# Kernel tuning notes

Hardware: AMD Instinct MI355X
Metric: run time of the kernel (lower is better)

Reference implementation:

```python
import jax, jax.numpy as jnp
import numpy as np

# ---- config (matches init_kwargs) ----
B, N, D = 16, 300, 256
HEADS, HD = 8, D // 8
FF = 1024
HID = FF // 2                      # SwiGLU hidden
SPATIAL = [(80, 80), (40, 40), (20, 20), (10, 10)]
LVL = len(SPATIAL)
NP = 4                              # points per level
TP = LVL * NP                       # total sampling points = 16
L = sum(h * w for h, w in SPATIAL)  # 8400
EPS = 1e-6


def setup_inputs() -> dict:
    key = jax.random.key(0)
    ks = jax.random.split(key, 24)
    s = 0.02
    return {
        "target": jax.random.normal(ks[0], (B, N, D), jnp.float32),
        "reference_points": jax.random.uniform(ks[1], (B, N, 1, 4), jnp.float32, 0.05, 0.95),
        "memory": jax.random.normal(ks[2], (B, L, D), jnp.float32),
        # self-attention
        "qkv_w": jax.random.normal(ks[3], (3 * D, D), jnp.float32) * s,
        "qkv_b": jnp.zeros((3 * D,), jnp.float32),
        "out_w": jax.random.normal(ks[4], (D, D), jnp.float32) * s,
        "out_b": jnp.zeros((D,), jnp.float32),
        "norm1_w": jnp.ones((D,), jnp.float32),
        # deformable cross-attention
        "off_w": jax.random.normal(ks[5], (HEADS * TP * 2, D), jnp.float32) * s,
        "off_b": jax.random.normal(ks[6], (HEADS * TP * 2,), jnp.float32) * 0.1,
        "aw_w": jax.random.normal(ks[7], (HEADS * TP, D), jnp.float32) * s,
        "aw_b": jnp.zeros((HEADS * TP,), jnp.float32),
        "cout_w": jax.random.normal(ks[8], (D, D), jnp.float32) * s,
        "cout_b": jnp.zeros((D,), jnp.float32),
        "norm2_w": jnp.ones((D,), jnp.float32),
        # SwiGLU FFN
        "w13": jax.random.normal(ks[9], (2 * HID, D), jnp.float32) * s,
        "w13_b": jnp.zeros((2 * HID,), jnp.float32),
        "w2": jax.random.normal(ks[10], (D, HID), jnp.float32) * s,
        "w2_b": jnp.zeros((D,), jnp.float32),
        "norm3_w": jnp.ones((D,), jnp.float32),
    }


def rmsnorm(x, w):
    return x * jax.lax.rsqrt(jnp.mean(x * x, axis=-1, keepdims=True) + EPS) * w


def bilinear_sample(vflat, loc, H, W):
    """vflat: (BH, hd, H*W); loc: (BH, Q, 2) in [0,1]. grid_sample align_corners=False, zero pad."""
    x = loc[..., 0] * W - 0.5
    y = loc[..., 1] * H - 0.5
    x0 = jnp.floor(x); y0 = jnp.floor(y)
    dx = x - x0; dy = y - y0
    x0i = x0.astype(jnp.int32); y0i = y0.astype(jnp.int32)

    def gather(xi, yi, w):
        valid = (xi >= 0) & (xi < W) & (yi >= 0) & (yi < H)
        idx = jnp.clip(yi, 0, H - 1) * W + jnp.clip(xi, 0, W - 1)
        g = jnp.take_along_axis(vflat, idx[:, None, :], axis=2)  # (BH, hd, Q)
        return g * (w * valid)[:, None, :]

    return (gather(x0i, y0i, (1 - dx) * (1 - dy))
            + gather(x0i + 1, y0i, dx * (1 - dy))
            + gather(x0i, y0i + 1, (1 - dx) * dy)
            + gather(x0i + 1, y0i + 1, dx * dy))


def reference(target, reference_points, memory, qkv_w, qkv_b, out_w, out_b, norm1_w,
              off_w, off_b, aw_w, aw_b, cout_w, cout_b, norm2_w,
              w13, w13_b, w2, w2_b, norm3_w):
    # ---------- self-attention (query_pos_embed=None, attn_mask=None) ----------
    qkv = target @ qkv_w.T + qkv_b                    # (B,N,3D)
    qkv = qkv.reshape(B, N, 3, HEADS, HD).transpose(2, 0, 3, 1, 4)
    q, k, v = qkv[0], qkv[1], qkv[2]                  # (B,H,N,hd)
    attn = jax.nn.softmax(jnp.einsum("bhqd,bhkd->bhqk", q, k) / np.sqrt(HD), axis=-1)
    sa = jnp.einsum("bhqk,bhkd->bhqd", attn, v).transpose(0, 2, 1, 3).reshape(B, N, D)
    x = rmsnorm(target + (sa @ out_w.T + out_b), norm1_w)

    # ---------- deformable cross-attention ----------
    # value_op: memory -> per-head value (B,H,hd,L)
    val = memory.reshape(B, L, HEADS, HD).transpose(0, 2, 3, 1).reshape(B * HEADS, HD, L)

    offsets = (x @ off_w.T + off_b).reshape(B, N, HEADS, TP, 2)
    aw = jax.nn.softmax((x @ aw_w.T + aw_b).reshape(B, N, HEADS, TP), axis=-1)

    ref_xy = reference_points[:, :, :, None, :2]      # (B,N,1,1,2)
    ref_wh = reference_points[:, :, :, None, 2:]
    pts_scale = 1.0 / NP
    loc = ref_xy + offsets * pts_scale * ref_wh * 0.5  # (B,N,H,TP,2)
    loc = loc.transpose(0, 2, 1, 3, 4).reshape(B * HEADS, N, TP, 2)

    sampled = []
    start = 0
    for li, (H, W) in enumerate(SPATIAL):
        v_l = jax.lax.dynamic_slice_in_dim(val, start, H * W, axis=2)
        loc_l = loc[:, :, li * NP:(li + 1) * NP, :].reshape(B * HEADS, N * NP, 2)
        s = bilinear_sample(v_l, loc_l, H, W).reshape(B * HEADS, HD, N, NP)
        sampled.append(s)
        start += H * W
    sampled = jnp.concatenate(sampled, axis=-1)        # (BH, hd, N, TP)

    w = aw.transpose(0, 2, 1, 3).reshape(B * HEADS, 1, N, TP)
    ca = (sampled * w).sum(-1)                         # (BH, hd, N)
    ca = ca.reshape(B, HEADS, HD, N).transpose(0, 3, 1, 2).reshape(B, N, D)
    ca = ca @ cout_w.T + cout_b

    x = rmsnorm(x + ca, norm2_w)

    # ---------- SwiGLU FFN ----------
    h = x @ w13.T + w13_b
    h1, h2 = h[..., :HID], h[..., HID:]
    ffn = (jax.nn.silu(h1) * h2) @ w2.T + w2_b
    x = jnp.clip(x + ffn, -65504.0, 65504.0)
    return rmsnorm(x, norm3_w)
```

## Files before the change

kernel.cpp:

```cpp
#include <hip/hip_runtime.h>
#include <cstdint>
#include <cstddef>


typedef __attribute__((ext_vector_type(8))) short bf16x8;
typedef __attribute__((ext_vector_type(4))) float f32x4;

__device__ __forceinline__ unsigned short f2bf(float f) {
  unsigned int u = __float_as_uint(f);
  u = (u + 0x7fffu + ((u >> 16) & 1u)) >> 16;
  return (unsigned short)u;
}
__device__ __forceinline__ unsigned int pack2bf(float lo, float hi) {
  return ((unsigned int)f2bf(hi) << 16) | (unsigned int)f2bf(lo);
}

__device__ __forceinline__ void gemm_dev(
    const float* __restrict__ A, const float* __restrict__ W,
    const float* __restrict__ bias, float* __restrict__ C,
    int N, int K, int row0, int col0,
    unsigned short* As, unsigned short* Ws)
{
  const int t = threadIdx.x, wave = t >> 6, lane = t & 63;
  const int lr = lane & 15, g = lane >> 4;
  const int sr = t >> 4, sc = (t & 15) * 4;

  float4 ra[4], rw[8];
  const float* Ab = A + (size_t)(row0 + sr) * K + sc;
  const float* Wb = W + (size_t)(col0 + sr) * K + sc;

#pragma unroll
  for (int i = 0; i < 4; ++i) ra[i] = *(const float4*)(Ab + (size_t)16 * i * K);
#pragma unroll
  for (int j = 0; j < 8; ++j) rw[j] = *(const float4*)(Wb + (size_t)16 * j * K);

  f32x4 acc[4][2] = {};

  for (int k0 = 0; k0 < K; k0 += 64) {
    __syncthreads();
#pragma unroll
    for (int i = 0; i < 4; ++i) {
      uint2 p;
      p.x = pack2bf(ra[i].x, ra[i].y);
      p.y = pack2bf(ra[i].z, ra[i].w);
      *(uint2*)&As[(sr + 16 * i) * 72 + sc] = p;
    }
#pragma unroll
    for (int j = 0; j < 8; ++j) {
      uint2 p;
      p.x = pack2bf(rw[j].x, rw[j].y);
      p.y = pack2bf(rw[j].z, rw[j].w);
      *(uint2*)&Ws[(sr + 16 * j) * 72 + sc] = p;
    }
    __syncthreads();

    if (k0 + 64 < K) {
#pragma unroll
      for (int i = 0; i < 4; ++i)
        ra[i] = *(const float4*)(Ab + (size_t)16 * i * K + k0 + 64);
#pragma unroll
      for (int j = 0; j < 8; ++j)
        rw[j] = *(const float4*)(Wb + (size_t)16 * j * K + k0 + 64);
    }

#pragma unroll
    for (int ks = 0; ks < 2; ++ks) {
      bf16x8 aA[4], bB[2];
#pragma unroll
      for (int i = 0; i < 4; ++i)
        aA[i] = *(const bf16x8*)&As[(i * 16 + lr) * 72 + ks * 32 + g * 8];
#pragma unroll
      for (int j = 0; j < 2; ++j)
        bB[j] = *(const bf16x8*)&Ws[(wave * 32 + j * 16 + lr) * 72 + ks * 32 + g * 8];
#pragma unroll
      for (int i = 0; i < 4; ++i)
#pragma unroll
        for (int j = 0; j < 2; ++j)
          acc[i][j] = __builtin_amdgcn_mfma_f32_16x16x32_bf16(aA[i], bB[j], acc[i][j], 0, 0, 0);
    }
  }

  const float b0 = bias[col0 + wave * 32 + lr];
  const float b1 = bias[col0 + wave * 32 + 16 + lr];
#pragma unroll
  for (int i = 0; i < 4; ++i) {
#pragma unroll
    for (int r = 0; r < 4; ++r) {
      const int row = row0 + i * 16 + g * 4 + r;
      float* dst = &C[(size_t)row * N + col0 + wave * 32 + lr];
      dst[0]  = acc[i][0][r] + b0;
      dst[16] = acc[i][1][r] + b1;
    }
  }
}

__global__ __launch_bounds__(256) void gemm_mfma(
    const float* __restrict__ A, const float* __restrict__ W,
    const float* __restrict__ bias, float* __restrict__ C, int N, int K)
{
  __shared__ __align__(16) unsigned short As[64 * 72];
  __shared__ __align__(16) unsigned short Ws[128 * 72];
  gemm_dev(A, W, bias, C, N, K, blockIdx.y * 64, blockIdx.x * 128, As, Ws);
}

__global__ __launch_bounds__(256) void gemm_offaw(
    const float* __restrict__ X,
    const float* __restrict__ off_w, const float* __restrict__ off_b, float* __restrict__ OF,
    const float* __restrict__ aw_w, const float* __restrict__ aw_b, float* __restrict__ AW,
    int K)
{
  __shared__ __align__(16) unsigned short As[64 * 72];
  __shared__ __align__(16) unsigned short Ws[128 * 72];
  if (blockIdx.x < 2)
    gemm_dev(X, off_w, off_b, OF, 256, K, blockIdx.y * 64, blockIdx.x * 128, As, Ws);
  else
    gemm_dev(X, aw_w, aw_b, AW, 128, K, blockIdx.y * 64, 0, As, Ws);
}

__global__ __launch_bounds__(256) void gemm_qkv(
    const float* __restrict__ A, const float* __restrict__ W,
    const float* __restrict__ bias,
    unsigned short* __restrict__ Qb, unsigned short* __restrict__ Kb,
    unsigned short* __restrict__ VTb)
{
  __shared__ __align__(16) unsigned short As[64 * 72];
  __shared__ __align__(16) unsigned short Ws[128 * 72];
  const int K = 256;
  const int t = threadIdx.x, wave = t >> 6, lane = t & 63;
  const int lr = lane & 15, g = lane >> 4;
  const int row0 = blockIdx.y * 64, col0 = blockIdx.x * 128;
  const int sr = t >> 4, sc = (t & 15) * 4;

  float4 ra[4], rw[8];
  const float* Ab = A + (size_t)(row0 + sr) * K + sc;
  const float* Wb = W + (size_t)(col0 + sr) * K + sc;

#pragma unroll
  for (int i = 0; i < 4; ++i) ra[i] = *(const float4*)(Ab + (size_t)16 * i * K);
#pragma unroll
  for (int j = 0; j < 8; ++j) rw[j] = *(const float4*)(Wb + (size_t)16 * j * K);

  f32x4 acc[4][2] = {};

  for (int k0 = 0; k0 < K; k0 += 64) {
    __syncthreads();
#pragma unroll
    for (int i = 0; i < 4; ++i) {
      uint2 p;
      p.x = pack2bf(ra[i].x, ra[i].y);
      p.y = pack2bf(ra[i].z, ra[i].w);
      *(uint2*)&As[(sr + 16 * i) * 72 + sc] = p;
    }
#pragma unroll
    for (int j = 0; j < 8; ++j) {
      uint2 p;
      p.x = pack2bf(rw[j].x, rw[j].y);
      p.y = pack2bf(rw[j].z, rw[j].w);
      *(uint2*)&Ws[(sr + 16 * j) * 72 + sc] = p;
    }
    __syncthreads();

    if (k0 + 64 < K) {
#pragma unroll
      for (int i = 0; i < 4; ++i)
        ra[i] = *(const float4*)(Ab + (size_t)16 * i * K + k0 + 64);
#pragma unroll
      for (int j = 0; j < 8; ++j)
        rw[j] = *(const float4*)(Wb + (size_t)16 * j * K + k0 + 64);
    }

#pragma unroll
    for (int ks = 0; ks < 2; ++ks) {
      bf16x8 aA[4], bB[2];
#pragma unroll
      for (int i = 0; i < 4; ++i)
        aA[i] = *(const bf16x8*)&As[(i * 16 + lr) * 72 + ks * 32 + g * 8];
#pragma unroll
      for (int j = 0; j < 2; ++j)
        bB[j] = *(const bf16x8*)&Ws[(wave * 32 + j * 16 + lr) * 72 + ks * 32 + g * 8];
#pragma unroll
      for (int i = 0; i < 4; ++i)
#pragma unroll
        for (int j = 0; j < 2; ++j)
          acc[i][j] = __builtin_amdgcn_mfma_f32_16x16x32_bf16(aA[i], bB[j], acc[i][j], 0, 0, 0);
    }
  }

  const int bx = blockIdx.x;
  const float scale = 0.17677669529663687f;
  const float b0 = bias[col0 + wave * 32 + lr];
  const float b1 = bias[col0 + wave * 32 + 16 + lr];

  if (bx < 4) {
    unsigned short* dstT = (bx < 2) ? Qb : Kb;
    const float mul = (bx < 2) ? scale : 1.0f;
#pragma unroll
    for (int i = 0; i < 4; ++i) {
#pragma unroll
      for (int r = 0; r < 4; ++r) {
        const int row = row0 + i * 16 + g * 4 + r;
        const int b = row / 300, n = row - b * 300;
#pragma unroll
        for (int j = 0; j < 2; ++j) {
          const int c768 = col0 + wave * 32 + j * 16 + lr;
          const int h = (c768 >> 5) & 7, c = c768 & 31;
          const float v = (acc[i][j][r] + (j ? b1 : b0)) * mul;
          dstT[((size_t)(b * 8 + h) * 304 + n) * 32 + c] = f2bf(v);
        }
      }
    }
  } else {
    __syncthreads();
#pragma unroll
    for (int i = 0; i < 4; ++i)
#pragma unroll
      for (int r = 0; r < 4; ++r)
#pragma unroll
        for (int j = 0; j < 2; ++j) {
          const int c_local = wave * 32 + j * 16 + lr;
          const int n_local = i * 16 + g * 4 + r;
          Ws[c_local * 72 + n_local] = f2bf(acc[i][j][r] + (j ? b1 : b0));
        }
    __syncthreads();
    for (int idx = t; idx < 128 * 64; idx += 256) {
      const int c_local = idx >> 6, n_local = idx & 63;
      const int row = row0 + n_local;
      const int b = row / 300, n = row - b * 300;
      const int c768 = col0 + c_local;
      const int h = (c768 >> 5) & 7, c = c768 & 31;
      VTb[((size_t)(b * 8 + h) * 32 + c) * 320 + n] = Ws[c_local * 72 + n_local];
    }
    if (blockIdx.y == 74) {
      for (int idx = t; idx < 64 * 32 * 20; idx += 256) {
        const int n = 300 + idx % 20;
        const int rem = idx / 20;
        const int c = rem & 31, bh4 = rem >> 5;
        const int b = bh4 >> 2, h = (bx - 4) * 4 + (bh4 & 3);
        VTb[((size_t)(b * 8 + h) * 32 + c) * 320 + n] = 0;
      }
    }
  }
}

__global__ __launch_bounds__(256) void gemm_swiglu(
    const float* __restrict__ Hb, const float* __restrict__ W,
    const float* __restrict__ bias, float* __restrict__ C)
{
  __shared__ __align__(16) unsigned short As[64 * 72];
  __shared__ __align__(16) unsigned short Ws[128 * 72];
  const int K = 512, N = 256;
  const int t = threadIdx.x, wave = t >> 6, lane = t & 63;
  const int lr = lane & 15, g = lane >> 4;
  const int row0 = blockIdx.y * 64, col0 = blockIdx.x * 128;
  const int sr = t >> 4, sc = (t & 15) * 4;

  float4 ra1[4], ra2[4], rw[8];
  const float* Ab = Hb + (size_t)(row0 + sr) * 1024 + sc;
  const float* Wb = W + (size_t)(col0 + sr) * K + sc;

#pragma unroll
  for (int i = 0; i < 4; ++i) {
    ra1[i] = *(const float4*)(Ab + (size_t)16 * i * 1024);
    ra2[i] = *(const float4*)(Ab + (size_t)16 * i * 1024 + 512);
  }
#pragma unroll
  for (int j = 0; j < 8; ++j) rw[j] = *(const float4*)(Wb + (size_t)16 * j * K);

  f32x4 acc[4][2] = {};

  for (int k0 = 0; k0 < K; k0 += 64) {
    __syncthreads();
#pragma unroll
    for (int i = 0; i < 4; ++i) {
      float4 v;
      v.x = ra1[i].x / (1.f + __expf(-ra1[i].x)) * ra2[i].x;
      v.y = ra1[i].y / (1.f + __expf(-ra1[i].y)) * ra2[i].y;
      v.z = ra1[i].z / (1.f + __expf(-ra1[i].z)) * ra2[i].z;
      v.w = ra1[i].w / (1.f + __expf(-ra1[i].w)) * ra2[i].w;
      uint2 p;
      p.x = pack2bf(v.x, v.y);
      p.y = pack2bf(v.z, v.w);
      *(uint2*)&As[(sr + 16 * i) * 72 + sc] = p;
    }
#pragma unroll
    for (int j = 0; j < 8; ++j) {
      uint2 p;
      p.x = pack2bf(rw[j].x, rw[j].y);
      p.y = pack2bf(rw[j].z, rw[j].w);
      *(uint2*)&Ws[(sr + 16 * j) * 72 + sc] = p;
    }
    __syncthreads();

    if (k0 + 64 < K) {
#pragma unroll
      for (int i = 0; i < 4; ++i) {
        ra1[i] = *(const float4*)(Ab + (size_t)16 * i * 1024 + k0 + 64);
        ra2[i] = *(const float4*)(Ab + (size_t)16 * i * 1024 + 512 + k0 + 64);
      }
#pragma unroll
      for (int j = 0; j < 8; ++j)
        rw[j] = *(const float4*)(Wb + (size_t)16 * j * K + k0 + 64);
    }

#pragma unroll
    for (int ks = 0; ks < 2; ++ks) {
      bf16x8 aA[4], bB[2];
#pragma unroll
      for (int i = 0; i < 4; ++i)
        aA[i] = *(const bf16x8*)&As[(i * 16 + lr) * 72 + ks * 32 + g * 8];
#pragma unroll
      for (int j = 0; j < 2; ++j)
        bB[j] = *(const bf16x8*)&Ws[(wave * 32 + j * 16 + lr) * 72 + ks * 32 + g * 8];
#pragma unroll
      for (int i = 0; i < 4; ++i)
#pragma unroll
        for (int j = 0; j < 2; ++j)
          acc[i][j] = __builtin_amdgcn_mfma_f32_16x16x32_bf16(aA[i], bB[j], acc[i][j], 0, 0, 0);
    }
  }

  const float b0 = bias[col0 + wave * 32 + lr];
  const float b1 = bias[col0 + wave * 32 + 16 + lr];
#pragma unroll
  for (int i = 0; i < 4; ++i) {
#pragma unroll
    for (int r = 0; r < 4; ++r) {
      const int row = row0 + i * 16 + g * 4 + r;
      float* dst = &C[(size_t)row * N + col0 + wave * 32 + lr];
      dst[0]  = acc[i][0][r] + b0;
      dst[16] = acc[i][1][r] + b1;
    }
  }
}

__global__ __launch_bounds__(64) void attn_core(
    const unsigned short* __restrict__ Qb, const unsigned short* __restrict__ Kb,
    const unsigned short* __restrict__ VTb, float* __restrict__ sa)
{
  __shared__ __align__(16) unsigned short P[16 * 40];
  const int gt = blockIdx.x;
  const int bh = blockIdx.y, b = bh >> 3, h = bh & 7;
  const int lane = threadIdx.x, lr = lane & 15, g = lane >> 4;

  const unsigned short* Kbase = Kb + (size_t)bh * 304 * 32;
  const unsigned short* Vbase = VTb + (size_t)bh * 32 * 320;

  bf16x8 aQ = *(const bf16x8*)&Qb[((size_t)bh * 304 + gt * 16 + lr) * 32 + g * 8];

  f32x4 s[19];
  const f32x4 zero = {0.f, 0.f, 0.f, 0.f};
#pragma unroll
  for (int kt = 0; kt < 19; ++kt) {
    bf16x8 bK = *(const bf16x8*)&Kbase[(kt * 16 + lr) * 32 + g * 8];
    s[kt] = __builtin_amdgcn_mfma_f32_16x16x32_bf16(aQ, bK, zero, 0, 0, 0);
  }
  if (lr >= 12) {
    s[18][0] = -1e30f; s[18][1] = -1e30f; s[18][2] = -1e30f; s[18][3] = -1e30f;
  }

  float inv[4];
#pragma unroll
  for (int r = 0; r < 4; ++r) {
    float m = -1e30f;
#pragma unroll
    for (int kt = 0; kt < 19; ++kt) m = fmaxf(m, s[kt][r]);
#pragma unroll
    for (int o = 8; o >= 1; o >>= 1) m = fmaxf(m, __shfl_xor(m, o));
    float sum = 0.f;
#pragma unroll
    for (int kt = 0; kt < 19; ++kt) {
      float e = __expf(s[kt][r] - m);
      s[kt][r] = e;
      sum += e;
    }
#pragma unroll
    for (int o = 8; o >= 1; o >>= 1) sum += __shfl_xor(sum, o);
    inv[r] = 1.f / sum;
  }

  f32x4 o0 = {0.f, 0.f, 0.f, 0.f}, o1 = {0.f, 0.f, 0.f, 0.f};
#pragma unroll
  for (int ks = 0; ks < 10; ++ks) {
#pragma unroll
    for (int tp = 0; tp < 2; ++tp) {
      const int kt = ks * 2 + tp;
#pragma unroll
      for (int r = 0; r < 4; ++r) {
        unsigned short pv = (kt < 19) ? f2bf(s[kt][r]) : (unsigned short)0;
        P[(g * 4 + r) * 40 + tp * 16 + lr] = pv;
      }
    }
    asm volatile("s_waitcnt lgkmcnt(0)" ::: "memory");
    __builtin_amdgcn_sched_barrier(0);
    bf16x8 aP = *(const bf16x8*)&P[lr * 40 + g * 8];
    bf16x8 bV0 = *(const bf16x8*)&Vbase[(size_t)lr * 320 + ks * 32 + g * 8];
    bf16x8 bV1 = *(const bf16x8*)&Vbase[(size_t)(16 + lr) * 320 + ks * 32 + g * 8];
    o0 = __builtin_amdgcn_mfma_f32_16x16x32_bf16(aP, bV0, o0, 0, 0, 0);
    o1 = __builtin_amdgcn_mfma_f32_16x16x32_bf16(aP, bV1, o1, 0, 0, 0);
  }

#pragma unroll
  for (int r = 0; r < 4; ++r) {
    const int q = gt * 16 + g * 4 + r;
    if (q < 300) {
      const float iv = inv[r];
      float* dst = &sa[((size_t)b * 300 + q) * 256 + h * 32];
      dst[lr] = o0[r] * iv;
      dst[16 + lr] = o1[r] * iv;
    }
  }
}

__global__ __launch_bounds__(256) void add_rmsnorm(
    const float* __restrict__ a, const float* __restrict__ bsrc,
    const float* __restrict__ w, float* __restrict__ out, int clip)
{
  __shared__ float red[4];
  const int row = blockIdx.x, t = threadIdx.x;
  const size_t idx = (size_t)row * 256 + t;
  float v = a[idx] + bsrc[idx];
  if (clip) v = fminf(fmaxf(v, -65504.f), 65504.f);
  float s = v * v;
#pragma unroll
  for (int o = 32; o; o >>= 1) s += __shfl_xor(s, o);
  if ((t & 63) == 0) red[t >> 6] = s;
  __syncthreads();
  float tot = red[0] + red[1] + red[2] + red[3];
  out[idx] = v * rsqrtf(tot * (1.0f / 256.0f) + 1e-6f) * w[t];
}

__global__ __launch_bounds__(256) void deform_k(
    const float* __restrict__ memory, const float* __restrict__ refp,
    const float* __restrict__ OFF, const float* __restrict__ AW,
    float* __restrict__ ca)
{
  __shared__ float locx[8][16], locy[8][16], wgt[8][16];
  const int bn = blockIdx.x, b = bn / 300, t = threadIdx.x;

  if (t < 128) {
    int h = t >> 4, p = t & 15;
    float cx = refp[(size_t)bn * 4 + 0], cy = refp[(size_t)bn * 4 + 1];
    float rw = refp[(size_t)bn * 4 + 2], rh = refp[(size_t)bn * 4 + 3];
    float ox = OFF[(size_t)bn * 256 + h * 32 + p * 2 + 0];
    float oy = OFF[(size_t)bn * 256 + h * 32 + p * 2 + 1];
    locx[h][p] = cx + ox * 0.125f * rw;
    locy[h][p] = cy + oy * 0.125f * rh;
    float av = AW[(size_t)bn * 128 + t];
    float mx = av;
#pragma unroll
    for (int o = 8; o; o >>= 1) mx = fmaxf(mx, __shfl_xor(mx, o));
    float e = __expf(av - mx);
    float ssum = e;
#pragma unroll
    for (int o = 8; o; o >>= 1) ssum += __shfl_xor(ssum, o);
    wgt[h][p] = e / ssum;
  }
  __syncthreads();

  const int h = t >> 5, hd = t & 31;
  const float* mb = memory + (size_t)b * 8500 * 256 + h * 32 + hd;
  float acc = 0.f;
#pragma unroll
  for (int p = 0; p < 16; ++p) {
    const int HWs[4] = {80, 40, 20, 10};
    const int Sts[4] = {0, 6400, 8000, 8400};
    const int li = p >> 2;
    const int Hh = HWs[li], Ww = HWs[li], st = Sts[li];
    float x = locx[h][p] * (float)Ww - 0.5f;
    float y = locy[h][p] * (float)Hh - 0.5f;
    float x0f = floorf(x), y0f = floorf(y);
    float dx = x - x0f, dy = y - y0f;
    int x0 = (int)x0f, y0 = (int)y0f;
    float awp = wgt[h][p];
#pragma unroll
    for (int cc = 0; cc < 4; ++cc) {
      int xi = x0 + (cc & 1), yi = y0 + (cc >> 1);
      float wc = ((cc & 1) ? dx : 1.f - dx) * ((cc >> 1) ? dy : 1.f - dy);
      bool valid = (xi >= 0) && (xi < Ww) && (yi >= 0) && (yi < Hh);
      int xc = xi < 0 ? 0 : (xi >= Ww ? Ww - 1 : xi);
      int yc = yi < 0 ? 0 : (yi >= Hh ? Hh - 1 : yi);
      float gv = mb[(size_t)(st + yc * Ww + xc) * 256];
      acc += gv * (valid ? wc * awp : 0.f);
    }
  }
  ca[(size_t)bn * 256 + t] = acc;
}

extern "C" void kernel_launch(void* const* d_in, const int* in_sizes, int n_in,
                              void* d_out, int out_size, void* d_ws, size_t ws_size,
                              hipStream_t stream)
{
  (void)in_sizes; (void)n_in; (void)out_size; (void)ws_size;
  const float* target  = (const float*)d_in[0];
  const float* refp    = (const float*)d_in[1];
  const float* memory  = (const float*)d_in[2];
  const float* qkv_w   = (const float*)d_in[3];
  const float* qkv_b   = (const float*)d_in[4];
  const float* out_w   = (const float*)d_in[5];
  const float* out_b   = (const float*)d_in[6];
  const float* norm1_w = (const float*)d_in[7];
  const float* off_w   = (const float*)d_in[8];
  const float* off_b   = (const float*)d_in[9];
  const float* aw_w    = (const float*)d_in[10];
  const float* aw_b    = (const float*)d_in[11];
  const float* cout_w  = (const float*)d_in[12];
  const float* cout_b  = (const float*)d_in[13];
  const float* norm2_w = (const float*)d_in[14];
  const float* w13     = (const float*)d_in[15];
  const float* w13_b   = (const float*)d_in[16];
  const float* w2      = (const float*)d_in[17];
  const float* w2_b    = (const float*)d_in[18];
  const float* norm3_w = (const float*)d_in[19];
  float* out = (float*)d_out;

  float* ws  = (float*)d_ws;
  float* SA  = ws;
  float* T1  = SA  + 4800 * 256;
  float* X   = T1  + 4800 * 256;
  float* OF  = X   + 4800 * 256;
  float* AWb = OF  + 4800 * 256;
  float* CA  = AWb + 4800 * 128;
  float* X2  = CA  + 4800 * 256;
  float* Hb  = X2  + 4800 * 256;
  unsigned short* Qb  = (unsigned short*)(Hb + 4800 * 1024);
  unsigned short* Kb  = Qb + 128 * 304 * 32;
  unsigned short* VTb = Kb + 128 * 304 * 32;

  dim3 blk(256);

  gemm_qkv<<<dim3(6, 75), blk, 0, stream>>>(target, qkv_w, qkv_b, Qb, Kb, VTb);
  attn_core<<<dim3(19, 128), dim3(64), 0, stream>>>(Qb, Kb, VTb, SA);
  gemm_mfma<<<dim3(2, 75), blk, 0, stream>>>(SA, out_w, out_b, T1, 256, 256);
  add_rmsnorm<<<4800, blk, 0, stream>>>(target, T1, norm1_w, X, 0);
  gemm_offaw<<<dim3(3, 75), blk, 0, stream>>>(X, off_w, off_b, OF, aw_w, aw_b, AWb, 256);
  deform_k<<<4800, blk, 0, stream>>>(memory, refp, OF, AWb, CA);
  gemm_mfma<<<dim3(2, 75), blk, 0, stream>>>(CA, cout_w, cout_b, T1, 256, 256);
  add_rmsnorm<<<4800, blk, 0, stream>>>(X, T1, norm2_w, X2, 0);
  gemm_mfma<<<dim3(8, 75), blk, 0, stream>>>(X2, w13, w13_b, Hb, 1024, 256);
  gemm_swiglu<<<dim3(2, 75), blk, 0, stream>>>(Hb, w2, w2_b, T1);
  add_rmsnorm<<<4800, blk, 0, stream>>>(X2, T1, norm3_w, out, 1);
}
```

Before: 136.3 us.

## Fuse residual add and RMSNorm into full-row GEMM epilogues

Adds a templated GEMM in which each block computes 32 full rows of 256 output columns. Its epilogue adds the bias and residual, reduces the sum of squares across waves through shared memory and applies RMSNorm directly. This replaces three GEMM+add_rmsnorm kernel pairs, removing three launches and the round trip of the intermediate T1 buffer. In exchange the grid shrinks from 150 blocks of 64x128 tiles to 150 blocks of 32x256 tiles, and each thread holds more weight registers, which could hurt occupancy.

```diff
diff --git a/kernel.cpp b/kernel.cpp
--- a/kernel.cpp
+++ b/kernel.cpp
@@ -115,6 +115,152 @@
     gemm_dev(X, off_w, off_b, OF, 256, K, blockIdx.y * 64, blockIdx.x * 128, As, Ws);
   else
     gemm_dev(X, aw_w, aw_b, AW, 128, K, blockIdx.y * 64, 0, As, Ws);
+}
+
+template <bool SWIGLU>
+__global__ __launch_bounds__(256) void gemm_rms32(
+    const float* __restrict__ A, const float* __restrict__ W,
+    const float* __restrict__ bias, const float* __restrict__ res,
+    const float* __restrict__ nw, float* __restrict__ C,
+    int K, int clip)
+{
+  __shared__ __align__(16) unsigned short As[32 * 72];
+  __shared__ __align__(16) unsigned short Ws[256 * 72];
+  __shared__ float rsum[32][4];
+
+  const int t = threadIdx.x, wave = t >> 6, lane = t & 63;
+  const int lr = lane & 15, g = lane >> 4;
+  const int row0 = blockIdx.x * 32;
+  const int sr = t >> 4, sc = (t & 15) * 4;
+  const int Astride = SWIGLU ? 1024 : K;
+
+  float4 ra1[2], ra2[2], rw[16];
+  const float* Ab = A + (size_t)(row0 + sr) * Astride + sc;
+  const float* Wb = W + (size_t)sr * K + sc;
+
+#pragma unroll
+  for (int i = 0; i < 2; ++i) {
+    ra1[i] = *(const float4*)(Ab + (size_t)16 * i * Astride);
+    if (SWIGLU) ra2[i] = *(const float4*)(Ab + (size_t)16 * i * Astride + 512);
+  }
+#pragma unroll
+  for (int j = 0; j < 16; ++j) rw[j] = *(const float4*)(Wb + (size_t)16 * j * K);
+
+  f32x4 acc[2][4] = {};
+
+  for (int k0 = 0; k0 < K; k0 += 64) {
+    __syncthreads();
+#pragma unroll
+    for (int i = 0; i < 2; ++i) {
+      float4 v;
+      if (SWIGLU) {
+        v.x = ra1[i].x / (1.f + __expf(-ra1[i].x)) * ra2[i].x;
+        v.y = ra1[i].y / (1.f + __expf(-ra1[i].y)) * ra2[i].y;
+        v.z = ra1[i].z / (1.f + __expf(-ra1[i].z)) * ra2[i].z;
+        v.w = ra1[i].w / (1.f + __expf(-ra1[i].w)) * ra2[i].w;
+      } else {
+        v = ra1[i];
+      }
+      uint2 p;
+      p.x = pack2bf(v.x, v.y);
+      p.y = pack2bf(v.z, v.w);
+      *(uint2*)&As[(sr + 16 * i) * 72 + sc] = p;
+    }
+#pragma unroll
+    for (int j = 0; j < 16; ++j) {
+      uint2 p;
+      p.x = pack2bf(rw[j].x, rw[j].y);
+      p.y = pack2bf(rw[j].z, rw[j].w);
+      *(uint2*)&Ws[(sr + 16 * j) * 72 + sc] = p;
+    }
+    __syncthreads();
+
+    if (k0 + 64 < K) {
+#pragma unroll
+      for (int i = 0; i < 2; ++i) {
+        ra1[i] = *(const float4*)(Ab + (size_t)16 * i * Astride + k0 + 64);
+        if (SWIGLU) ra2[i] = *(const float4*)(Ab + (size_t)16 * i * Astride + 512 + k0 + 64);
+      }
+#pragma unroll
+      for (int j = 0; j < 16; ++j)
+        rw[j] = *(const float4*)(Wb + (size_t)16 * j * K + k0 + 64);
+    }
+
+#pragma unroll
+    for (int ks = 0; ks < 2; ++ks) {
+      bf16x8 aA[2], bB[4];
+#pragma unroll
+      for (int i = 0; i < 2; ++i)
+        aA[i] = *(const bf16x8*)&As[(i * 16 + lr) * 72 + ks * 32 + g * 8];
+#pragma unroll
+      for (int j = 0; j < 4; ++j)
+        bB[j] = *(const bf16x8*)&Ws[(wave * 64 + j * 16 + lr) * 72 + ks * 32 + g * 8];
+#pragma unroll
+      for (int i = 0; i < 2; ++i)
+#pragma unroll
+        for (int j = 0; j < 4; ++j)
+          acc[i][j] = __builtin_amdgcn_mfma_f32_16x16x32_bf16(aA[i], bB[j], acc[i][j], 0, 0, 0);
+    }
+  }
+
+  float bj[4], wj[4];
+#pragma unroll
+  for (int j = 0; j < 4; ++j) {
+    bj[j] = bias[wave * 64 + j * 16 + lr];
+    wj[j] = nw[wave * 64 + j * 16 + lr];
+  }
+
+  float part[2][4] = {};
+#pragma unroll
+  for (int i = 0; i < 2; ++i) {
+#pragma unroll
+    for (int r = 0; r < 4; ++r) {
+      const int row = row0 + i * 16 + g * 4 + r;
+#pragma unroll
+      for (int j = 0; j < 4; ++j) {
+        const int col = wave * 64 + j * 16 + lr;
+        float v = acc[i][j][r] + bj[j] + res[(size_t)row * 256 + col];
+        if (clip) v = fminf(fmaxf(v, -65504.f), 65504.f);
+        acc[i][j][r] = v;
+        part[i][r] += v * v;
+      }
+    }
+  }
+#pragma unroll
+  for (int i = 0; i < 2; ++i)
+#pragma unroll
+    for (int r = 0; r < 4; ++r) {
+      float s = part[i][r];
+      s += __shfl_xor(s, 1);
+      s += __shfl_xor(s, 2);
+      s += __shfl_xor(s, 4);
+      s += __shfl_xor(s, 8);
+      part[i][r] = s;
+    }
+  if (lr == 0) {
+#pragma unroll
+    for (int i = 0; i < 2; ++i)
+#pragma unroll
+      for (int r = 0; r < 4; ++r)
+        rsum[i * 16 + g * 4 + r][wave] = part[i][r];
+  }
+  __syncthreads();
+
+#pragma unroll
+  for (int i = 0; i < 2; ++i) {
+#pragma unroll
+    for (int r = 0; r < 4; ++r) {
+      const int row = row0 + i * 16 + g * 4 + r;
+      const f32x4 q = *(const f32x4*)&rsum[i * 16 + g * 4 + r][0];
+      const float tot = q[0] + q[1] + q[2] + q[3];
+      const float scale = rsqrtf(tot * (1.0f / 256.0f) + 1e-6f);
+#pragma unroll
+      for (int j = 0; j < 4; ++j) {
+        const int col = wave * 64 + j * 16 + lr;
+        C[(size_t)row * 256 + col] = acc[i][j][r] * scale * wj[j];
+      }
+    }
+  }
 }
 
 __global__ __launch_bounds__(256) void gemm_qkv(
@@ -242,97 +388,6 @@
   }
 }
 
-__global__ __launch_bounds__(256) void gemm_swiglu(
-    const float* __restrict__ Hb, const float* __restrict__ W,
-    const float* __restrict__ bias, float* __restrict__ C)
-{
-  __shared__ __align__(16) unsigned short As[64 * 72];
-  __shared__ __align__(16) unsigned short Ws[128 * 72];
-  const int K = 512, N = 256;
-  const int t = threadIdx.x, wave = t >> 6, lane = t & 63;
-  const int lr = lane & 15, g = lane >> 4;
-  const int row0 = blockIdx.y * 64, col0 = blockIdx.x * 128;
-  const int sr = t >> 4, sc = (t & 15) * 4;
-
-  float4 ra1[4], ra2[4], rw[8];
-  const float* Ab = Hb + (size_t)(row0 + sr) * 1024 + sc;
-  const float* Wb = W + (size_t)(col0 + sr) * K + sc;
-
-#pragma unroll
-  for (int i = 0; i < 4; ++i) {
-    ra1[i] = *(const float4*)(Ab + (size_t)16 * i * 1024);
-    ra2[i] = *(const float4*)(Ab + (size_t)16 * i * 1024 + 512);
-  }
-#pragma unroll
-  for (int j = 0; j < 8; ++j) rw[j] = *(const float4*)(Wb + (size_t)16 * j * K);
-
-  f32x4 acc[4][2] = {};
-
-  for (int k0 = 0; k0 < K; k0 += 64) {
-    __syncthreads();
-#pragma unroll
-    for (int i = 0; i < 4; ++i) {
-      float4 v;
-      v.x = ra1[i].x / (1.f + __expf(-ra1[i].x)) * ra2[i].x;
-      v.y = ra1[i].y / (1.f + __expf(-ra1[i].y)) * ra2[i].y;
-      v.z = ra1[i].z / (1.f + __expf(-ra1[i].z)) * ra2[i].z;
-      v.w = ra1[i].w / (1.f + __expf(-ra1[i].w)) * ra2[i].w;
-      uint2 p;
-      p.x = pack2bf(v.x, v.y);
-      p.y = pack2bf(v.z, v.w);
-      *(uint2*)&As[(sr + 16 * i) * 72 + sc] = p;
-    }
-#pragma unroll
-    for (int j = 0; j < 8; ++j) {
-      uint2 p;
-      p.x = pack2bf(rw[j].x, rw[j].y);
-      p.y = pack2bf(rw[j].z, rw[j].w);
-      *(uint2*)&Ws[(sr + 16 * j) * 72 + sc] = p;
-    }
-    __syncthreads();
-
-    if (k0 + 64 < K) {
-#pragma unroll
-      for (int i = 0; i < 4; ++i) {
-        ra1[i] = *(const float4*)(Ab + (size_t)16 * i * 1024 + k0 + 64);
-        ra2[i] = *(const float4*)(Ab + (size_t)16 * i * 1024 + 512 + k0 + 64);
-      }
-#pragma unroll
-      for (int j = 0; j < 8; ++j)
-        rw[j] = *(const float4*)(Wb + (size_t)16 * j * K + k0 + 64);
-    }
-
-#pragma unroll
-    for (int ks = 0; ks < 2; ++ks) {
-      bf16x8 aA[4], bB[2];
-#pragma unroll
-      for (int i = 0; i < 4; ++i)
-        aA[i] = *(const bf16x8*)&As[(i * 16 + lr) * 72 + ks * 32 + g * 8];
-#pragma unroll
-      for (int j = 0; j < 2; ++j)
-        bB[j] = *(const bf16x8*)&Ws[(wave * 32 + j * 16 + lr) * 72 + ks * 32 + g * 8];
-#pragma unroll
-      for (int i = 0; i < 4; ++i)
-#pragma unroll
-        for (int j = 0; j < 2; ++j)
-          acc[i][j] = __builtin_amdgcn_mfma_f32_16x16x32_bf16(aA[i], bB[j], acc[i][j], 0, 0, 0);
-    }
-  }
-
-  const float b0 = bias[col0 + wave * 32 + lr];
-  const float b1 = bias[col0 + wave * 32 + 16 + lr];
-#pragma unroll
-  for (int i = 0; i < 4; ++i) {
-#pragma unroll
-    for (int r = 0; r < 4; ++r) {
-      const int row = row0 + i * 16 + g * 4 + r;
-      float* dst = &C[(size_t)row * N + col0 + wave * 32 + lr];
-      dst[0]  = acc[i][0][r] + b0;
-      dst[16] = acc[i][1][r] + b1;
-    }
-  }
-}
-
 __global__ __launch_bounds__(64) void attn_core(
     const unsigned short* __restrict__ Qb, const unsigned short* __restrict__ Kb,
     const unsigned short* __restrict__ VTb, float* __restrict__ sa)
@@ -409,24 +464,6 @@
       dst[16 + lr] = o1[r] * iv;
     }
   }
-}
-
-__global__ __launch_bounds__(256) void add_rmsnorm(
-    const float* __restrict__ a, const float* __restrict__ bsrc,
-    const float* __restrict__ w, float* __restrict__ out, int clip)
-{
-  __shared__ float red[4];
-  const int row = blockIdx.x, t = threadIdx.x;
-  const size_t idx = (size_t)row * 256 + t;
-  float v = a[idx] + bsrc[idx];
-  if (clip) v = fminf(fmaxf(v, -65504.f), 65504.f);
-  float s = v * v;
-#pragma unroll
-  for (int o = 32; o; o >>= 1) s += __shfl_xor(s, o);
-  if ((t & 63) == 0) red[t >> 6] = s;
-  __syncthreads();
-  float tot = red[0] + red[1] + red[2] + red[3];
-  out[idx] = v * rsqrtf(tot * (1.0f / 256.0f) + 1e-6f) * w[t];
 }
 
 __global__ __launch_bounds__(256) void deform_k(
@@ -515,8 +552,7 @@
 
   float* ws  = (float*)d_ws;
   float* SA  = ws;
-  float* T1  = SA  + 4800 * 256;
-  float* X   = T1  + 4800 * 256;
+  float* X   = SA  + 4800 * 256;
   float* OF  = X   + 4800 * 256;
   float* AWb = OF  + 4800 * 256;
   float* CA  = AWb + 4800 * 128;
@@ -530,13 +566,10 @@
 
   gemm_qkv<<<dim3(6, 75), blk, 0, stream>>>(target, qkv_w, qkv_b, Qb, Kb, VTb);
   attn_core<<<dim3(19, 128), dim3(64), 0, stream>>>(Qb, Kb, VTb, SA);
-  gemm_mfma<<<dim3(2, 75), blk, 0, stream>>>(SA, out_w, out_b, T1, 256, 256);
-  add_rmsnorm<<<4800, blk, 0, stream>>>(target, T1, norm1_w, X, 0);
+  gemm_rms32<false><<<150, blk, 0, stream>>>(SA, out_w, out_b, target, norm1_w, X, 256, 0);
   gemm_offaw<<<dim3(3, 75), blk, 0, stream>>>(X, off_w, off_b, OF, aw_w, aw_b, AWb, 256);
   deform_k<<<4800, blk, 0, stream>>>(memory, refp, OF, AWb, CA);
-  gemm_mfma<<<dim3(2, 75), blk, 0, stream>>>(CA, cout_w, cout_b, T1, 256, 256);
-  add_rmsnorm<<<4800, blk, 0, stream>>>(X, T1, norm2_w, X2, 0);
+  gemm_rms32<false><<<150, blk, 0, stream>>>(CA, cout_w, cout_b, X, norm2_w, X2, 256, 0);
   gemm_mfma<<<dim3(8, 75), blk, 0, stream>>>(X2, w13, w13_b, Hb, 1024, 256);
-  gemm_swiglu<<<dim3(2, 75), blk, 0, stream>>>(Hb, w2, w2_b, T1);
-  add_rmsnorm<<<4800, blk, 0, stream>>>(X2, T1, norm3_w, out, 1);
-}
+  gemm_rms32<true><<<150, blk, 0, stream>>>(Hb, w2, w2_b, X2, norm3_w, out, 512, 1);
+}
```

Result: faster. 131.0 us (-3.9%).
